# Performance work log

Hardware: AMD Instinct MI355X
Metric: run time of the kernel (lower is better)

## Reference

```python
import jax, jax.numpy as jnp
import numpy as np

B, MODEL_DIM, HIGH_DIM, T, KEEP = 8, 1024, 2048, 4096, 64


def setup_inputs() -> dict:
    key = jax.random.key(0)
    k1, k2, k3, k4, k5 = jax.random.split(key, 5)
    x = jax.random.normal(k1, (B, MODEL_DIM, T), dtype=jnp.float32)
    # conv1d kernel-size-1 weights == dense matrices; torch default uniform init
    s_e = 1.0 / np.sqrt(MODEL_DIM)
    W_e = jax.random.uniform(k2, (HIGH_DIM, MODEL_DIM), jnp.float32, -s_e, s_e)
    b_e = jax.random.uniform(k3, (HIGH_DIM,), jnp.float32, -s_e, s_e)
    s_c = 1.0 / np.sqrt(HIGH_DIM)
    W_c = jax.random.uniform(k4, (MODEL_DIM, HIGH_DIM), jnp.float32, -s_c, s_c)
    b_c = jax.random.uniform(k5, (MODEL_DIM,), jnp.float32, -s_c, s_c)
    return {"x": x, "W_e": W_e, "b_e": b_e, "W_c": W_c, "b_c": b_c}


def reference(x, W_e, b_e, W_c, b_c):
    # expand: 1x1 conv == per-timestep GEMM  [B,C,T] -> [B,D,T]
    y = jnp.einsum('bct,dc->bdt', x, W_e) + b_e[None, :, None]
    # top-k along time axis per (batch, channel) row; keep only those entries
    vals, idx = jax.lax.top_k(y, KEEP)            # [B,D,KEEP]
    sparse = jnp.zeros_like(y).at[
        jnp.arange(B)[:, None, None],
        jnp.arange(HIGH_DIM)[None, :, None],
        idx,
    ].set(vals)                                   # [B,D,T] sparse activation
    # contract: 1x1 conv back to model_dim
    out = jnp.einsum('bdt,md->bmt', sparse, W_c) + b_c[None, :, None]
    return (out, sparse)
```

## Files before the change

### kernel.cpp

```cpp
#include <hip/hip_runtime.h>
#include <hip/hip_bf16.h>
#include <stdint.h>

#define B_    8
#define MD    1024
#define HD    2048
#define T_    4096
#define KEEP_ 64
#define CAP   96
#define BANDW 5e-3f
#define AMB   2e-6
#define NCAND 512

typedef __attribute__((ext_vector_type(8))) short short8;
typedef __attribute__((ext_vector_type(4))) float f32x4;
typedef __attribute__((ext_vector_type(8))) _Float16 half8;

__device__ __forceinline__ void gload_lds16(const void* g, void* l) {
    __builtin_amdgcn_global_load_lds(
        (const __attribute__((address_space(1))) uint32_t*)g,
        (__attribute__((address_space(3))) uint32_t*)l, 16, 0, 0);
}

__device__ __forceinline__ short f2h(float a) {
    _Float16 h = (_Float16)a;
    short s;
    __builtin_memcpy(&s, &h, 2);
    return s;
}

__device__ __forceinline__ float h2f(short s) {
    _Float16 h;
    __builtin_memcpy(&h, &s, 2);
    return (float)h;
}

__device__ __forceinline__ void split1h(float a, short& h, short& l) {
    _Float16 hh = (_Float16)a;
    float r = a - (float)hh;
    h = f2h(a);
    l = f2h(r);
    (void)hh;
}

__device__ __forceinline__ uint32_t sortable(float f) {
    uint32_t u = __float_as_uint(f);
    return (u & 0x80000000u) ? ~u : (u | 0x80000000u);
}

__global__ void k_transpose_wc(const float* __restrict__ Wc,
                               __hip_bfloat16* __restrict__ WcT) {
    __shared__ float s[32][33];
    const int d0 = blockIdx.x * 32;
    const int m0 = blockIdx.y * 32;
    const int tx = threadIdx.x;
    const int ty = threadIdx.y;
    #pragma unroll
    for (int k = 0; k < 4; k++)
        s[ty + k * 8][tx] = Wc[(size_t)(m0 + ty + k * 8) * HD + d0 + tx];
    __syncthreads();
    #pragma unroll
    for (int k = 0; k < 4; k++)
        WcT[(size_t)(d0 + ty + k * 8) * MD + m0 + tx] =
            __float2bfloat16(s[tx][ty + k * 8]);
}

__global__ void k_round_we(const float* __restrict__ We,
                           short* __restrict__ hi) {
    const int i = (blockIdx.x * 256 + threadIdx.x) * 4;
    float4 v = *(const float4*)&We[i];
    short4 h;
    h.x = f2h(v.x);
    h.y = f2h(v.y);
    h.z = f2h(v.z);
    h.w = f2h(v.w);
    *(short4*)&hi[i] = h;
}

__global__ void k_split_x(const float* __restrict__ x,
                          short* __restrict__ xTh, short* __restrict__ xTl) {
    __shared__ float s[32][33];
    const int t0 = blockIdx.x * 32;
    const int c0 = blockIdx.y * 32;
    const int b  = blockIdx.z;
    const int tx = threadIdx.x;
    const int ty = threadIdx.y;
    const float* xb = x + (size_t)b * MD * T_;
    #pragma unroll
    for (int k = 0; k < 4; k++)
        s[ty + k * 8][tx] = xb[(size_t)(c0 + ty + k * 8) * T_ + t0 + tx];
    __syncthreads();
    const int id = ty * 32 + tx;
    const int tl = id >> 3;
    const int c4 = (id & 7) * 4;
    short4 h4, l4;
    split1h(s[c4 + 0][tl], h4.x, l4.x);
    split1h(s[c4 + 1][tl], h4.y, l4.y);
    split1h(s[c4 + 2][tl], h4.z, l4.z);
    split1h(s[c4 + 3][tl], h4.w, l4.w);
    const size_t o = ((size_t)b * T_ + t0 + tl) * MD + c0 + c4;
    *(short4*)&xTh[o] = h4;
    *(short4*)&xTl[o] = l4;
}

__launch_bounds__(256)
__global__ void k_gemm_mfma(const short* __restrict__ xTh,
                            const short* __restrict__ Weh,
                            const float* __restrict__ be,
                            float* __restrict__ y) {
    __shared__ __align__(16) short Ah[128 * 32];
    __shared__ __align__(16) short Bh[128 * 32];

    const int t0  = blockIdx.x * 128;
    const int d0  = blockIdx.y * 128;
    const int b   = blockIdx.z;
    const int tid = threadIdx.x;
    const int lane = tid & 63;
    const int wave = tid >> 6;
    const int wm = wave >> 1, wn = wave & 1;
    const int fm = lane & 15, fq = lane >> 4;

    const short* A_h = Weh + (size_t)d0 * MD;
    const short* B_h = xTh + ((size_t)b * T_ + t0) * MD;

    f32x4 acc[4][4];
    #pragma unroll
    for (int i = 0; i < 4; i++)
        #pragma unroll
        for (int j = 0; j < 4; j++) acc[i][j] = (f32x4)0.f;

    for (int k0 = 0; k0 < MD; k0 += 32) {
        #pragma unroll
        for (int i = 0; i < 2; i++) {
            const int e   = i * 256 + tid;
            const int row = e >> 2, kc = (e & 3) << 3;
            const size_t go = (size_t)row * MD + k0 + kc;
            const int lo = e << 3;
            gload_lds16(A_h + go, &Ah[lo]);
            gload_lds16(B_h + go, &Bh[lo]);
        }
        __syncthreads();

        half8 ah[4], bh[4];
        #pragma unroll
        for (int mt = 0; mt < 4; mt++) {
            const int r = wm * 64 + mt * 16 + fm;
            ah[mt] = *(const half8*)&Ah[r * 32 + fq * 8];
        }
        #pragma unroll
        for (int nt = 0; nt < 4; nt++) {
            const int r = wn * 64 + nt * 16 + fm;
            bh[nt] = *(const half8*)&Bh[r * 32 + fq * 8];
        }
        #pragma unroll
        for (int mt = 0; mt < 4; mt++)
            #pragma unroll
            for (int nt = 0; nt < 4; nt++)
                acc[mt][nt] = __builtin_amdgcn_mfma_f32_16x16x32_f16(
                    ah[mt], bh[nt], acc[mt][nt], 0, 0, 0);
        __syncthreads();
    }

    _Float16* yh = (_Float16*)y;
    #pragma unroll
    for (int mt = 0; mt < 4; mt++) {
        #pragma unroll
        for (int r = 0; r < 4; r++) {
            const int d = d0 + wm * 64 + mt * 16 + fq * 4 + r;
            const float bias = be[d];
            _Float16* yd = yh + ((size_t)b * HD + d) * (2 * T_)
                              + t0 + wn * 64 + fm;
            #pragma unroll
            for (int nt = 0; nt < 4; nt++)
                yd[nt * 16] = (_Float16)(acc[mt][nt][r] + bias);
        }
    }
}

__launch_bounds__(256)
__global__ void k_topk(float* __restrict__ y,
                       const float* __restrict__ x,
                       const float* __restrict__ We,
                       const float* __restrict__ be,
                       const short* __restrict__ xTh,
                       const short* __restrict__ xTl,
                       int* __restrict__ colcnt, float2* __restrict__ collist) {
    __shared__ double s_redd[256];
    __shared__ float  s_fred[8];
    __shared__ int    s_ired[8];
    __shared__ unsigned long long s_ck[NCAND];
    __shared__ int s_n;
    __shared__ uint32_t s_Vu;
    __shared__ int s_bidx[64];
    __shared__ double s_bval[64];
    __shared__ unsigned char s_bkeep[64];
    __shared__ int s_nhi, s_nb, s_flag;

    const int row  = blockIdx.x;
    const int b    = row >> 11;
    const int d    = row & 2047;
    const int tid  = threadIdx.x;
    const int lane = tid & 63;
    const int wave = tid >> 6;
    float* yrow = y + (size_t)row * T_;

    const short* yrow16 = (const short*)yrow;
    short8 r0 = *(const short8*)&yrow16[(size_t)tid * 8];
    short8 r1 = *(const short8*)&yrow16[(size_t)(256 + tid) * 8];
    float fv[16];
    #pragma unroll
    for (int e = 0; e < 8; e++) { fv[e] = h2f(r0[e]); fv[8 + e] = h2f(r1[e]); }

    float s1 = 0.f, s2 = 0.f;
    #pragma unroll
    for (int q = 0; q < 16; q++) { s1 += fv[q]; s2 = fmaf(fv[q], fv[q], s2); }
    for (int off = 32; off > 0; off >>= 1) {
        s1 += __shfl_down(s1, off);
        s2 += __shfl_down(s2, off);
    }
    if (lane == 0) { s_fred[wave] = s1; s_fred[4 + wave] = s2; }
    __syncthreads();
    const float S1 = s_fred[0] + s_fred[1] + s_fred[2] + s_fred[3];
    const float S2 = s_fred[4] + s_fred[5] + s_fred[6] + s_fred[7];
    const float mu = S1 * (1.f / T_);
    const float sd = sqrtf(fmaxf(S2 * (1.f / T_) - mu * mu, 1e-20f));

    float thr = mu + 2.0f * sd;
    int total = 0;
    for (int iter = 0; iter < 16; iter++) {
        int c = 0;
        #pragma unroll
        for (int q = 0; q < 16; q++) c += (fv[q] >= thr);
        for (int off = 32; off > 0; off >>= 1) c += __shfl_down(c, off);
        __syncthreads();
        if (lane == 0) s_ired[wave] = c;
        __syncthreads();
        total = s_ired[0] + s_ired[1] + s_ired[2] + s_ired[3];
        if (total >= KEEP_ && total <= NCAND) break;
        thr += (total < KEEP_) ? (-0.25f * sd) : (0.25f * sd);
    }

    if (tid == 0) { s_n = 0; s_Vu = 0; }
    __syncthreads();
    #pragma unroll
    for (int q = 0; q < 16; q++) {
        if (fv[q] >= thr) {
            const int i = (q < 8) ? (tid * 8 + q) : (2048 + tid * 8 + (q - 8));
            const int pos = atomicAdd(&s_n, 1);
            if (pos < NCAND)
                s_ck[pos] = ((unsigned long long)sortable(fv[q]) << 32) |
                            (uint32_t)(~i);
        }
    }
    __syncthreads();
    int nc = min(s_n, NCAND);

    for (int ci = tid; ci < nc; ci += 256) {
        const unsigned long long k = s_ck[ci];
        int r = 0;
        for (int j = 0; j < nc; j++) r += (s_ck[j] > k);
        if (r == KEEP_ - 1) s_Vu = (uint32_t)(k >> 32);
    }
    __syncthreads();
    const uint32_t Vu = s_Vu;
    const uint32_t Vb = (Vu & 0x80000000u) ? (Vu & 0x7FFFFFFFu) : ~Vu;
    const float Vf = __uint_as_float(Vb);
    const float hi_thr = Vf + BANDW;
    const float lo_thr = Vf - BANDW;
    const uint32_t hiU = sortable(hi_thr);
    const uint32_t loU = sortable(lo_thr);

    if (lo_thr < thr) {
        __syncthreads();
        if (tid == 0) s_n = 0;
        __syncthreads();
        #pragma unroll
        for (int q = 0; q < 16; q++) {
            if (fv[q] >= lo_thr) {
                const int i = (q < 8) ? (tid * 8 + q)
                                      : (2048 + tid * 8 + (q - 8));
                const int pos = atomicAdd(&s_n, 1);
                if (pos < NCAND)
                    s_ck[pos] = ((unsigned long long)sortable(fv[q]) << 32) |
                                (uint32_t)(~i);
            }
        }
        __syncthreads();
        nc = min(s_n, NCAND);
    }

    if (tid == 0) { s_nhi = 0; s_nb = 0; }
    __syncthreads();
    for (int ci = tid; ci < nc; ci += 256) {
        const unsigned long long k = s_ck[ci];
        const uint32_t u = (uint32_t)(k >> 32);
        if (u > hiU) {
            atomicAdd(&s_nhi, 1);
        } else if (u >= loU) {
            const int p = atomicAdd(&s_nb, 1);
            if (p < 64) s_bidx[p] = (int)(~(uint32_t)k & 0xFFFFu);
        }
    }
    __syncthreads();
    const int nb    = min(s_nb, 64);
    const int slots = KEEP_ - s_nhi;

    if (nb > slots) {
        const int c0l = lane * 16;
        const float* wrow = We + (size_t)d * MD;
        for (int j = wave; j < nb; j += 4) {
            const int t = s_bidx[j];
            const size_t xo = ((size_t)b * T_ + t) * MD + c0l;
            double acc = 0.0;
            #pragma unroll
            for (int qq = 0; qq < 4; qq++) {
                const float4 w4 = *(const float4*)&wrow[c0l + qq * 4];
                const short4 h4 = *(const short4*)&xTh[xo + qq * 4];
                const short4 l4 = *(const short4*)&xTl[xo + qq * 4];
                acc += (double)w4.x * (double)(h2f(h4.x) + h2f(l4.x));
                acc += (double)w4.y * (double)(h2f(h4.y) + h2f(l4.y));
                acc += (double)w4.z * (double)(h2f(h4.z) + h2f(l4.z));
                acc += (double)w4.w * (double)(h2f(h4.w) + h2f(l4.w));
            }
            #pragma unroll
            for (int off = 32; off > 0; off >>= 1)
                acc += __shfl_down(acc, off);
            if (lane == 0) s_bval[j] = acc + (double)be[d];
        }
        __syncthreads();
        if (tid < nb) {
            const double v = s_bval[tid];
            const int    ti = s_bidx[tid];
            int rank = 0;
            for (int j = 0; j < nb; j++) {
                if (j == tid) continue;
                if (s_bval[j] > v ||
                    (s_bval[j] == v && s_bidx[j] < ti)) rank++;
            }
            s_bkeep[tid] = (rank < slots) ? 1 : 0;
        }
        __syncthreads();
        if (tid == 0) {
            double kmin = 1e300, dmax = -1e300;
            for (int j = 0; j < nb; j++) {
                if (s_bkeep[j]) { if (s_bval[j] < kmin) kmin = s_bval[j]; }
                else            { if (s_bval[j] > dmax) dmax = s_bval[j]; }
            }
            s_flag = (kmin - dmax < AMB) ? 1 : 0;
        }
        __syncthreads();
        if (s_flag) {
            for (int j = 0; j < nb; j++) {
                const int t = s_bidx[j];
                double partial = 0.0;
                for (int c = tid; c < MD; c += 256)
                    partial += (double)We[(size_t)d * MD + c] *
                               (double)x[((size_t)b * MD + c) * T_ + t];
                s_redd[tid] = partial;
                __syncthreads();
                for (int off = 128; off > 0; off >>= 1) {
                    if (tid < off) s_redd[tid] += s_redd[tid + off];
                    __syncthreads();
                }
                if (tid == 0) s_bval[j] = s_redd[0] + (double)be[d];
                __syncthreads();
            }
            if (tid < nb) {
                const double v = s_bval[tid];
                const int    ti = s_bidx[tid];
                int rank = 0;
                for (int j = 0; j < nb; j++) {
                    if (j == tid) continue;
                    if (s_bval[j] > v ||
                        (s_bval[j] == v && s_bidx[j] < ti)) rank++;
                }
                s_bkeep[tid] = (rank < slots) ? 1 : 0;
            }
        }
    } else {
        if (tid < nb) s_bkeep[tid] = 1;
    }
    __syncthreads();

    #pragma unroll
    for (int jj = 0; jj < 2; jj++) {
        float buf[8];
        #pragma unroll
        for (int e = 0; e < 8; e++) {
            const int q = jj * 8 + e;
            const int i = jj * 2048 + tid * 8 + e;
            const float f = fv[q];
            const uint32_t u = sortable(f);
            bool keep;
            if (u > hiU) {
                keep = true;
            } else if (u < loU) {
                keep = false;
            } else {
                keep = false;
                for (int p = 0; p < nb; p++)
                    if (s_bidx[p] == i) { keep = (s_bkeep[p] != 0); break; }
            }
            if (keep) {
                const int col = b * T_ + i;
                const int pos = atomicAdd(&colcnt[col], 1);
                if (pos < CAP)
                    collist[(size_t)col * CAP + pos] =
                        make_float2(__int_as_float(d), f);
                buf[e] = f;
            } else {
                buf[e] = 0.0f;
            }
        }
        float* base = yrow + jj * 2048 + (size_t)tid * 8;
        *(float4*)(base)     = make_float4(buf[0], buf[1], buf[2], buf[3]);
        *(float4*)(base + 4) = make_float4(buf[4], buf[5], buf[6], buf[7]);
    }
}

__launch_bounds__(256)
__global__ void k_contract(const int* __restrict__ colcnt,
                           const float2* __restrict__ collist,
                           const __hip_bfloat16* __restrict__ WcT,
                           const float* __restrict__ bc,
                           float* __restrict__ out) {
    __shared__ float2 s_list[16][CAP];
    __shared__ int    s_cnt[16];
    __shared__ float  s_t[256][17];

    const int t0  = blockIdx.x * 16;
    const int b   = blockIdx.y;
    const int tid = threadIdx.x;

    if (tid < 16) s_cnt[tid] = min(colcnt[b * T_ + t0 + tid], CAP);
    __syncthreads();
    for (int c = 0; c < 16; c++) {
        const int n = s_cnt[c];
        for (int i = tid; i < n; i += 256)
            s_list[c][i] = collist[(size_t)(b * T_ + t0 + c) * CAP + i];
    }
    __syncthreads();

    for (int mc = 0; mc < 4; mc++) {
        const int m = mc * 256 + tid;
        const float bias = bc[m];
        float acc[16];
        #pragma unroll
        for (int c = 0; c < 16; c++) acc[c] = bias;

        #pragma unroll
        for (int c = 0; c < 16; c++) {
            const int n = s_cnt[c];
            float a = acc[c];
            int i = 0;
            for (; i + 4 <= n; i += 4) {
                const float2 e0 = s_list[c][i + 0];
                const float2 e1 = s_list[c][i + 1];
                const float2 e2 = s_list[c][i + 2];
                const float2 e3 = s_list[c][i + 3];
                const float w0 = __bfloat162float(
                    WcT[(size_t)__float_as_int(e0.x) * MD + m]);
                const float w1 = __bfloat162float(
                    WcT[(size_t)__float_as_int(e1.x) * MD + m]);
                const float w2 = __bfloat162float(
                    WcT[(size_t)__float_as_int(e2.x) * MD + m]);
                const float w3 = __bfloat162float(
                    WcT[(size_t)__float_as_int(e3.x) * MD + m]);
                a = fmaf(e0.y, w0, a);
                a = fmaf(e1.y, w1, a);
                a = fmaf(e2.y, w2, a);
                a = fmaf(e3.y, w3, a);
            }
            for (; i < n; i++) {
                const float2 e = s_list[c][i];
                const float w = __bfloat162float(
                    WcT[(size_t)__float_as_int(e.x) * MD + m]);
                a = fmaf(e.y, w, a);
            }
            acc[c] = a;
        }

        #pragma unroll
        for (int c = 0; c < 16; c++) s_t[tid][c] = acc[c];
        __syncthreads();
        #pragma unroll
        for (int pass = 0; pass < 4; pass++) {
            const int r  = pass * 64 + (tid >> 2);
            const int cj = (tid & 3) * 4;
            float4 v;
            v.x = s_t[r][cj + 0];
            v.y = s_t[r][cj + 1];
            v.z = s_t[r][cj + 2];
            v.w = s_t[r][cj + 3];
            const int m_out = mc * 256 + r;
            *(float4*)&out[((size_t)b * MD + m_out) * T_ + t0 + cj] = v;
        }
        __syncthreads();
    }
}

extern "C" void kernel_launch(void* const* d_in, const int* in_sizes, int n_in,
                              void* d_out, int out_size, void* d_ws, size_t ws_size,
                              hipStream_t stream) {
    const float* x  = (const float*)d_in[0];
    const float* We = (const float*)d_in[1];
    const float* be = (const float*)d_in[2];
    const float* Wc = (const float*)d_in[3];
    const float* bc = (const float*)d_in[4];

    float* out0 = (float*)d_out;
    float* out1 = out0 + (size_t)B_ * MD * T_;

    char* ws = (char*)d_ws;
    int*     colcnt  = (int*)ws;
    float2*  collist = (float2*)(ws + (size_t)B_ * T_ * sizeof(int));
    __hip_bfloat16* WcT =
        (__hip_bfloat16*)(ws + (size_t)B_ * T_ * sizeof(int) +
                          (size_t)B_ * T_ * CAP * sizeof(float2));

    short* xTh = (short*)out0;
    short* xTl = xTh + (size_t)B_ * T_ * MD;
    short* Weh = (short*)collist;

    hipMemsetAsync(colcnt, 0, (size_t)B_ * T_ * sizeof(int), stream);

    k_transpose_wc<<<dim3(HD / 32, MD / 32), dim3(32, 8), 0, stream>>>(Wc, WcT);
    k_round_we<<<(HD * MD) / 1024, 256, 0, stream>>>(We, Weh);
    k_split_x<<<dim3(T_ / 32, MD / 32, B_), dim3(32, 8), 0, stream>>>(x, xTh, xTl);
    k_gemm_mfma<<<dim3(T_ / 128, HD / 128, B_), 256, 0, stream>>>(
        xTh, Weh, be, out1);
    k_topk<<<B_ * HD, 256, 0, stream>>>(out1, x, We, be, xTh, xTl,
                                        colcnt, collist);
    k_contract<<<dim3(T_ / 16, B_), 256, 0, stream>>>(colcnt, collist, WcT, bc, out0);
}
```

Before: 1.167 ms.

## Vectorize contract kernel: four output rows per thread with 8-byte weight loads

The sparse contract kernel now has each thread own four consecutive output rows (m) instead of looping over four 256-row chunks. It reads four bf16 weights in one 8-byte load per sparse entry and amortizes each LDS list read across four FMAs. Outputs are written directly as float4 over four time columns, which removes the shared-memory transpose and its barriers. In exchange the per-thread global loads are strided 8 bytes per lane, and each time-column store now touches four rows instead of being coalesced across threads.

```diff
diff --git a/kernel.cpp b/kernel.cpp
--- a/kernel.cpp
+++ b/kernel.cpp
@@ -426,14 +426,15 @@
                            float* __restrict__ out) {
     __shared__ float2 s_list[16][CAP];
     __shared__ int    s_cnt[16];
-    __shared__ float  s_t[256][17];
 
     const int t0  = blockIdx.x * 16;
     const int b   = blockIdx.y;
     const int tid = threadIdx.x;
+    const int m4  = tid * 4;
 
     if (tid < 16) s_cnt[tid] = min(colcnt[b * T_ + t0 + tid], CAP);
     __syncthreads();
+    #pragma unroll
     for (int c = 0; c < 16; c++) {
         const int n = s_cnt[c];
         for (int i = tid; i < n; i += 256)
@@ -441,61 +442,52 @@
     }
     __syncthreads();
 
-    for (int mc = 0; mc < 4; mc++) {
-        const int m = mc * 256 + tid;
-        const float bias = bc[m];
-        float acc[16];
-        #pragma unroll
-        for (int c = 0; c < 16; c++) acc[c] = bias;
-
-        #pragma unroll
-        for (int c = 0; c < 16; c++) {
-            const int n = s_cnt[c];
-            float a = acc[c];
-            int i = 0;
-            for (; i + 4 <= n; i += 4) {
-                const float2 e0 = s_list[c][i + 0];
-                const float2 e1 = s_list[c][i + 1];
-                const float2 e2 = s_list[c][i + 2];
-                const float2 e3 = s_list[c][i + 3];
-                const float w0 = __bfloat162float(
-                    WcT[(size_t)__float_as_int(e0.x) * MD + m]);
-                const float w1 = __bfloat162float(
-                    WcT[(size_t)__float_as_int(e1.x) * MD + m]);
-                const float w2 = __bfloat162float(
-                    WcT[(size_t)__float_as_int(e2.x) * MD + m]);
-                const float w3 = __bfloat162float(
-                    WcT[(size_t)__float_as_int(e3.x) * MD + m]);
-                a = fmaf(e0.y, w0, a);
-                a = fmaf(e1.y, w1, a);
-                a = fmaf(e2.y, w2, a);
-                a = fmaf(e3.y, w3, a);
-            }
-            for (; i < n; i++) {
-                const float2 e = s_list[c][i];
-                const float w = __bfloat162float(
-                    WcT[(size_t)__float_as_int(e.x) * MD + m]);
-                a = fmaf(e.y, w, a);
-            }
-            acc[c] = a;
-        }
-
-        #pragma unroll
-        for (int c = 0; c < 16; c++) s_t[tid][c] = acc[c];
-        __syncthreads();
-        #pragma unroll
-        for (int pass = 0; pass < 4; pass++) {
-            const int r  = pass * 64 + (tid >> 2);
-            const int cj = (tid & 3) * 4;
-            float4 v;
-            v.x = s_t[r][cj + 0];
-            v.y = s_t[r][cj + 1];
-            v.z = s_t[r][cj + 2];
-            v.w = s_t[r][cj + 3];
-            const int m_out = mc * 256 + r;
-            *(float4*)&out[((size_t)b * MD + m_out) * T_ + t0 + cj] = v;
-        }
-        __syncthreads();
+    const float4 bias4 = *(const float4*)&bc[m4];
+    const char* wbase = (const char*)WcT + (size_t)m4 * 2;
+
+    auto dot_col = [&](int c, f32x4& a) {
+        const int n = s_cnt[c];
+        int i = 0;
+        for (; i + 2 <= n; i += 2) {
+            const float2 e0 = s_list[c][i];
+            const float2 e1 = s_list[c][i + 1];
+            const uint2 w0 = *(const uint2*)(wbase +
+                ((size_t)(uint32_t)__float_as_int(e0.x) << 11));
+            const uint2 w1 = *(const uint2*)(wbase +
+                ((size_t)(uint32_t)__float_as_int(e1.x) << 11));
+            a[0] = fmaf(e0.y, __uint_as_float(w0.x << 16), a[0]);
+            a[1] = fmaf(e0.y, __uint_as_float(w0.x & 0xffff0000u), a[1]);
+            a[2] = fmaf(e0.y, __uint_as_float(w0.y << 16), a[2]);
+            a[3] = fmaf(e0.y, __uint_as_float(w0.y & 0xffff0000u), a[3]);
+            a[0] = fmaf(e1.y, __uint_as_float(w1.x << 16), a[0]);
+            a[1] = fmaf(e1.y, __uint_as_float(w1.x & 0xffff0000u), a[1]);
+            a[2] = fmaf(e1.y, __uint_as_float(w1.y << 16), a[2]);
+            a[3] = fmaf(e1.y, __uint_as_float(w1.y & 0xffff0000u), a[3]);
+        }
+        if (i < n) {
+            const float2 e0 = s_list[c][i];
+            const uint2 w0 = *(const uint2*)(wbase +
+                ((size_t)(uint32_t)__float_as_int(e0.x) << 11));
+            a[0] = fmaf(e0.y, __uint_as_float(w0.x << 16), a[0]);
+            a[1] = fmaf(e0.y, __uint_as_float(w0.x & 0xffff0000u), a[1]);
+            a[2] = fmaf(e0.y, __uint_as_float(w0.y << 16), a[2]);
+            a[3] = fmaf(e0.y, __uint_as_float(w0.y & 0xffff0000u), a[3]);
+        }
+    };
+
+    const f32x4 binit = {bias4.x, bias4.y, bias4.z, bias4.w};
+
+    for (int cg = 0; cg < 4; cg++) {
+        f32x4 a0 = binit, a1 = binit, a2 = binit, a3 = binit;
+        dot_col(cg * 4 + 0, a0);
+        dot_col(cg * 4 + 1, a1);
+        dot_col(cg * 4 + 2, a2);
+        dot_col(cg * 4 + 3, a3);
+        #pragma unroll
+        for (int j = 0; j < 4; j++) {
+            float4 v = make_float4(a0[j], a1[j], a2[j], a3[j]);
+            *(float4*)&out[((size_t)b * MD + m4 + j) * T_ + t0 + cg * 4] = v;
+        }
     }
 }
 
```

Result: slower. 1.196 ms (+2.4%).
